# Kernel optimization log

Measured on AMD Instinct MI355X. Metric: run time of the kernel, lower is better.

Reference implementation:

```python
import jax, jax.numpy as jnp
import numpy as np

B, T, L, D, H = 4, 8, 197, 512, 8
DK = D // H
SIM_TH = 0.0
N = T * (L - 1)  # 1568 local tokens

def _ln(x, g, b, eps=1e-5):
    x32 = x.astype(jnp.float32)
    m = jnp.mean(x32, axis=-1, keepdims=True)
    v = jnp.mean((x32 - m) ** 2, axis=-1, keepdims=True)
    return (((x32 - m) * jax.lax.rsqrt(v + eps)) * g + b).astype(x.dtype)

def _qgelu(x):
    return x * jax.nn.sigmoid(1.702 * x)

def _mha(x, w_in, b_in, w_out, b_out):
    # torch nn.MultiheadAttention, x: [S, Bt, D] (seq-first)
    S, Bt, _ = x.shape
    qkv = x @ w_in.T + b_in
    q, k, v = jnp.split(qkv, 3, axis=-1)
    q = q.reshape(S, Bt, H, DK); k = k.reshape(S, Bt, H, DK); v = v.reshape(S, Bt, H, DK)
    scores = jnp.einsum('sbhd,tbhd->bhst', q, k) / jnp.sqrt(jnp.asarray(DK, x.dtype))
    p = jax.nn.softmax(scores, axis=-1)
    o = jnp.einsum('bhst,tbhd->sbhd', p, v).reshape(S, Bt, D)
    return o @ w_out.T + b_out

def _resblock(x, ln1g, ln1b, inw, inb, outw, outb, ln2g, ln2b, fcw, fcb, pw, pb):
    x = x + _mha(_ln(x, ln1g, ln1b), inw, inb, outw, outb)
    h = _qgelu(_ln(x, ln2g, ln2b) @ fcw.T + fcb)
    return x + h @ pw.T + pb

def _build_graph(x, g_mask):
    xd = jax.lax.stop_gradient(x)  # matches x.detach()
    xn = xd / jnp.maximum(jnp.linalg.norm(xd, axis=-1, keepdims=True), 1e-12)
    sim = jnp.einsum('bnd,bmd->bnm', xn, xn)
    adj = jnp.where(sim < SIM_TH, 0.0, sim)
    return adj * g_mask  # t != 1 branch

def _graph_attn(x, mask, wq, bq, wk, bk, wv, bv, wo, bo):
    Bb, Nn, _ = x.shape
    def heads(a):
        return a.reshape(Bb, Nn, H, DK).transpose(0, 2, 1, 3)
    Q = heads(x @ wq.T + bq); K = heads(x @ wk.T + bk); V = heads(x @ wv.T + bv)
    scores = jnp.einsum('bhnd,bhmd->bhnm', Q, K) / jnp.sqrt(jnp.asarray(DK, x.dtype))
    m = mask[:, None]  # [b,1,N,N]
    scores = jnp.where(m == 0, -jnp.inf, scores * m)  # scores*mask then masked_fill(mask==0,-inf)
    p = jax.nn.softmax(scores, axis=-1)
    o = jnp.einsum('bhnm,bhmd->bhnd', p, V).transpose(0, 2, 1, 3).reshape(Bb, Nn, D)
    return o @ wo.T + bo

def _forward(x, proj_w, proj_b,
             m_ln1g, m_ln1b, m_inw, m_inb, m_outw, m_outb,
             m_ln2g, m_ln2b, m_fcw, m_fcb, m_pw, m_pb,
             g_wq, g_bq, g_wk, g_bk, g_wv, g_bv, g_wo, g_bo,
             ln1g, ln1b, a_inw, a_inb, a_outw, a_outb,
             ln2g, ln2b, fcw, fcb, pw, pb, g_mask):
    b, t, l, d = x.shape
    x = x @ proj_w.T + proj_b
    glob = x[:, :, 0, :].transpose(1, 0, 2)  # [t,b,d]
    msg = (m_ln1g, m_ln1b, m_inw, m_inb, m_outw, m_outb, m_ln2g, m_ln2b, m_fcw, m_fcb, m_pw, m_pb)
    glob = _resblock(glob, *msg)
    glob = _resblock(glob, *msg)  # message_attn applied twice (shared weights)
    glob = glob.reshape(1, t, b, d)
    loc = x[:, :, 1:, :].reshape(b, t * (l - 1), d)
    gm = _build_graph(loc, g_mask)
    loc = _graph_attn(loc, gm, g_wq, g_bq, g_wk, g_bk, g_wv, g_bv, g_wo, g_bo)
    loc = loc.reshape(b, t, l - 1, d).transpose(2, 1, 0, 3)  # [l-1,t,b,d]
    y = jnp.concatenate([glob, loc], axis=0).reshape(l, t * b, d)
    y = y + _mha(_ln(y, ln1g, ln1b), a_inw, a_inb, a_outw, a_outb)
    y = y + _qgelu(_ln(y, ln2g, ln2b) @ fcw.T + fcb) @ pw.T + pb
    return y.reshape(l, t, b, d).transpose(2, 1, 0, 3)  # [b,t,l,d]

def setup_inputs() -> dict:
    key = jax.random.key(0)
    ks = jax.random.split(key, 64)
    s = 0.02
    def w(i, shape):
        return jax.random.normal(ks[i], shape, jnp.float32) * s
    ones = jnp.ones((D,), jnp.float32); zeros = jnp.zeros((D,), jnp.float32)
    gm = (jax.random.uniform(ks[60], (N, N)) < 0.5).astype(jnp.float32)
    gm = gm.at[jnp.arange(N), jnp.arange(N)].set(1.0)  # keep self-edges so no row is fully masked
    return dict(
        x=jax.random.normal(ks[0], (B, T, L, D), jnp.float32),
        proj_w=w(1, (D, D)), proj_b=jnp.zeros((D,), jnp.float32),
        m_ln1g=ones, m_ln1b=zeros,
        m_inw=w(2, (3 * D, D)), m_inb=jnp.zeros((3 * D,), jnp.float32),
        m_outw=w(3, (D, D)), m_outb=zeros,
        m_ln2g=ones, m_ln2b=zeros,
        m_fcw=w(4, (4 * D, D)), m_fcb=jnp.zeros((4 * D,), jnp.float32),
        m_pw=w(5, (D, 4 * D)), m_pb=zeros,
        g_wq=w(6, (D, D)), g_bq=zeros, g_wk=w(7, (D, D)), g_bk=zeros,
        g_wv=w(8, (D, D)), g_bv=zeros, g_wo=w(9, (D, D)), g_bo=zeros,
        ln1g=ones, ln1b=zeros,
        a_inw=w(10, (3 * D, D)), a_inb=jnp.zeros((3 * D,), jnp.float32),
        a_outw=w(11, (D, D)), a_outb=zeros,
        ln2g=ones, ln2b=zeros,
        fcw=w(12, (4 * D, D)), fcb=jnp.zeros((4 * D,), jnp.float32),
        pw=w(13, (D, 4 * D)), pb=zeros,
        g_mask=gm,
    )

def reference(x, proj_w, proj_b, m_ln1g, m_ln1b, m_inw, m_inb, m_outw, m_outb,
              m_ln2g, m_ln2b, m_fcw, m_fcb, m_pw, m_pb,
              g_wq, g_bq, g_wk, g_bk, g_wv, g_bv, g_wo, g_bo,
              ln1g, ln1b, a_inw, a_inb, a_outw, a_outb,
              ln2g, ln2b, fcw, fcb, pw, pb, g_mask):
    return _forward(x, proj_w, proj_b, m_ln1g, m_ln1b, m_inw, m_inb, m_outw, m_outb,
                    m_ln2g, m_ln2b, m_fcw, m_fcb, m_pw, m_pb,
                    g_wq, g_bq, g_wk, g_bk, g_wv, g_bv, g_wo, g_bo,
                    ln1g, ln1b, a_inw, a_inb, a_outw, a_outb,
                    ln2g, ln2b, fcw, fcb, pw, pb, g_mask)
```

## Files before the change

kernel.cpp:

```cpp
#include <hip/hip_runtime.h>
#include <hip/hip_bf16.h>

typedef unsigned short u16;
typedef __attribute__((ext_vector_type(8))) short bf16x8;
typedef __attribute__((ext_vector_type(4))) float f32x4;

#define FINF __builtin_huge_valf()

static __device__ __forceinline__ float bf2f(u16 v){ union{unsigned u; float f;} c; c.u = ((unsigned)v)<<16; return c.f; }
static __device__ __forceinline__ u16 f2bf(float f){ union{__hip_bfloat16 h; u16 u;} c; c.h = __float2bfloat16(f); return c.u; }
static __device__ __forceinline__ bf16x8 scale8(bf16x8 v, float s){
  bf16x8 o;
  #pragma unroll
  for (int e=0;e<8;e++) o[e] = (short)f2bf(bf2f((u16)v[e])*s);
  return o;
}

static __device__ __forceinline__ void gload16(const void* g, void* l){
  __builtin_amdgcn_global_load_lds(
      (const __attribute__((address_space(1))) void*)g,
      (__attribute__((address_space(3))) void*)l, 16, 0, 0);
}

#define WAIT_VM0()   { asm volatile("s_waitcnt vmcnt(0)" ::: "memory"); __builtin_amdgcn_sched_barrier(0); }
#define BARRIER()    { __builtin_amdgcn_sched_barrier(0); __builtin_amdgcn_s_barrier(); __builtin_amdgcn_sched_barrier(0); }

struct CvtArgs {
  const float* src[14];
  u16* dst[14];
  int n[14];
};
__global__ __launch_bounds__(256) void cvt_multi(CvtArgs a){
  int seg = blockIdx.y;
  const float* s = a.src[seg]; u16* d = a.dst[seg]; int n = a.n[seg];
  for (int i = (blockIdx.x*256 + threadIdx.x)*4; i < n; i += gridDim.x*256*4){
    float4 v = *(const float4*)(s + i);
    ushort4 o = { f2bf(v.x), f2bf(v.y), f2bf(v.z), f2bf(v.w) };
    *(ushort4*)(d + i) = o;
  }
}

__global__ __launch_bounds__(256) void concat_bias(const float* a, const float* b, const float* c, float* o){
  int i = blockIdx.x*256 + threadIdx.x;
  o[i] = i < 512 ? a[i] : (i < 1024 ? b[i-512] : c[i-1024]);
}

template<int BM, int EPI, int MW>
__global__ __launch_bounds__(256,MW) void gemm_nt(
    const u16* __restrict__ A, const u16* __restrict__ Bw,
    const float* __restrict__ bias, const float* aux, void* out,
    int M, int Nn, int K, int ldc, long aBatch, long bBatch, long cBatch)
{
  constexpr int MI = BM/32;
  constexpr int WSPAN = BM/2;
  __shared__ __align__(16) u16 a_lds[2*BM*64];
  __shared__ __align__(16) u16 b_lds[2*128*64];
  const int z = blockIdx.z;
  const u16* Az = A + (long)z*aBatch;
  const u16* Bz = Bw + (long)z*bBatch;
  const int n0 = blockIdx.x*128, m0 = blockIdx.y*BM;
  const int t = threadIdx.x, lane = t & 63, wave = t >> 6;
  const int wr = wave >> 1, wc = wave & 1;
  const int r = lane & 15, kq = lane >> 4;

  const int srow = t >> 3;
  const int scol = ((t&7)*8) ^ ((srow&7)<<3);
  int rowA[MI], rowB[4];
  #pragma unroll
  for (int i=0;i<MI;i++){ int ga = m0 + i*32 + srow; rowA[i] = ga < M ? ga : M-1; }
  #pragma unroll
  for (int i=0;i<4;i++){ int gb = n0 + i*32 + srow; rowB[i] = gb < Nn ? gb : Nn-1; }

  f32x4 acc[MI][4] = {};
  const int nkt = K >> 6;

  auto STAGE = [&](int kt, int buf){
    const long koff = (long)kt*64 + scol;
    #pragma unroll
    for (int i=0;i<MI;i++)
      gload16(Az + (long)rowA[i]*K + koff, (char*)a_lds + buf*(BM*128) + i*4096 + wave*1024);
    #pragma unroll
    for (int i=0;i<4;i++)
      gload16(Bz + (long)rowB[i]*K + koff, (char*)b_lds + buf*16384 + i*4096 + wave*1024);
  };

  STAGE(0,0);
  WAIT_VM0(); BARRIER();
  for (int kt=0; kt<nkt; kt++){
    const int cur = kt&1;
    if (kt+1 < nkt) STAGE(kt+1, cur^1);
    const u16* al = a_lds + cur*BM*64;
    const u16* bl = b_lds + cur*8192;
    #pragma unroll
    for (int kk=0; kk<2; kk++){
      bf16x8 af[MI], bfr[4];
      #pragma unroll
      for (int i=0;i<MI;i++){
        int rw = wr*WSPAN + i*16 + r;
        af[i] = *(const bf16x8*)&al[rw*64 + ((kk*32 + kq*8) ^ ((rw&7)<<3))];
      }
      #pragma unroll
      for (int j=0;j<4;j++){
        int rw = wc*64 + j*16 + r;
        bfr[j] = *(const bf16x8*)&bl[rw*64 + ((kk*32 + kq*8) ^ ((rw&7)<<3))];
      }
      #pragma unroll
      for (int i=0;i<MI;i++)
        #pragma unroll
        for (int j=0;j<4;j++)
          acc[i][j] = __builtin_amdgcn_mfma_f32_16x16x32_bf16(af[i], bfr[j], acc[i][j], 0,0,0);
    }
    WAIT_VM0(); BARRIER();
  }

  #pragma unroll
  for (int i=0;i<MI;i++){
    #pragma unroll
    for (int j=0;j<4;j++){
      int gcol = n0 + wc*64 + j*16 + r;
      if (gcol >= Nn) continue;
      float bv = bias ? bias[gcol] : 0.f;
      #pragma unroll
      for (int rr=0; rr<4; rr++){
        int grow = m0 + wr*WSPAN + i*16 + kq*4 + rr;
        if (grow >= M) continue;
        float v = acc[i][j][rr] + bv;
        if constexpr (EPI==0){
          ((float*)out)[(long)z*cBatch + (long)grow*ldc + gcol] = v;
        } else if constexpr (EPI==1){
          ((u16*)out)[(long)z*cBatch + (long)grow*ldc + gcol] = f2bf(v);
        } else if constexpr (EPI==2){
          long idx = (long)z*cBatch + (long)grow*ldc + gcol;
          ((float*)out)[idx] = aux[idx] + v;
        } else if constexpr (EPI==3){
          float g = v / (1.f + __expf(-1.702f*v));
          ((u16*)out)[(long)z*cBatch + (long)grow*ldc + gcol] = f2bf(g);
        } else if constexpr (EPI==4){
          float adj = v < 0.f ? 0.f : v;
          float gmv = aux[(long)grow*Nn + gcol];
          ((u16*)out)[(long)z*cBatch + (long)grow*ldc + gcol] = f2bf(adj*gmv);
        } else if constexpr (EPI==5){
          int b = grow/1568, n = grow%1568, tt = n/196, lp = n%196;
          int yrow = (1+lp)*32 + tt*4 + b;
          ((float*)out)[(long)yrow*ldc + gcol] = v;
        } else if constexpr (EPI==6){
          long idx = (long)grow*ldc + gcol;
          int l = grow>>5, rb = grow&31, tt = rb>>2, bb = rb&3;
          ((float*)out)[((long)((bb*8+tt)*197) + l)*512 + gcol] = aux[idx] + v;
        }
      }
    }
  }
}

__global__ __launch_bounds__(256) void transpose_v(
    const u16* __restrict__ src, u16* __restrict__ vt,
    int nrows, long zofs, long nofs, int vcol0, int outld)
{
  __shared__ u16 tile[64][66];
  const int t = threadIdx.x;
  const int nt = blockIdx.x, h = blockIdx.y, z = blockIdx.z;
  const int n0 = nt*64;
  const int rlo = t>>3, c0 = (t&7)*8;
  #pragma unroll
  for (int i=0;i<2;i++){
    int nl = i*32 + rlo;
    int n = n0 + nl; int nc = n < nrows ? n : nrows-1;
    const u16* s = src + (long)z*zofs + (long)nc*nofs + vcol0 + h*64 + c0;
    uint4 v = *(const uint4*)s;
    bool dead = n >= nrows;
    #pragma unroll
    for (int e=0;e<8;e++) tile[nl][c0+e] = dead ? (u16)0 : ((const u16*)&v)[e];
  }
  __syncthreads();
  #pragma unroll
  for (int i=0;i<2;i++){
    int d = i*32 + rlo;
    u16 tmp[8];
    #pragma unroll
    for (int e=0;e<8;e++) tmp[e] = tile[c0+e][d];
    int ncol = n0 + c0;
    if (ncol + 8 <= outld){
      u16* dst = vt + ((long)((z*8+h)*64 + d))*outld + ncol;
      *(uint4*)dst = *(uint4*)tmp;
    }
  }
}

template<bool MASKED>
__global__ __launch_bounds__(256,4) void flash3(
    const u16* __restrict__ QKV, const u16* __restrict__ VT,
    const u16* __restrict__ gmask, u16* __restrict__ Out,
    int nq, int nk, int nqb, long qBatch, long qRow,
    long oBatch, long oRow, long gmBatch, int vtld)
{
  __shared__ __align__(16) u16 k_lds[2*4096];
  __shared__ __align__(16) u16 p_lds[4][1024];
  int h, z, qb;
  if constexpr (MASKED){
    int id = blockIdx.x;
    int a = id>>6, c = id&7; h = (id>>3)&7;
    int G = a*8 + c;
    if (G >= 4*nqb) return;
    z = G / nqb; qb = G % nqb;
  } else {
    qb = blockIdx.x; h = blockIdx.y; z = blockIdx.z;
  }
  const int t = threadIdx.x, lane = t&63, wave = t>>6;
  const int r = lane&15, kq = lane>>4;
  const u16* Qb = QKV + (long)z*qBatch + h*64;
  const u16* Kb = Qb + 512;
  const u16* Vt = VT + (long)(z*8+h)*64*vtld;
  const int qt0 = qb*64;
  const int q0  = qt0 + wave*16;
  const int q   = q0 + r;
  const int qc  = q < nq ? q : nq-1;
  const u16* Gq = MASKED ? (gmask + (long)z*gmBatch + (long)qc*nk) : nullptr;

  bf16x8 qf0, qf1;
  { const u16* qp = Qb + (long)qc*qRow + kq*8;
    qf0 = scale8(*(const bf16x8*)qp, 0.125f);
    qf1 = scale8(*(const bf16x8*)(qp+32), 0.125f); }

  const int srow = t>>3;
  const int scol = ((t&7)*8) ^ ((srow&7)<<3);

  auto stage_k = [&](int kt, int buf){
    #pragma unroll
    for (int i=0;i<2;i++){
      int j = kt*64 + i*32 + srow; if (j > nk-1) j = nk-1;
      gload16(Kb + (long)j*qRow + scol, (char*)k_lds + buf*8192 + i*4096 + wave*1024);
    }
  };

  bf16x8 ONES;
  #pragma unroll
  for (int e=0;e<8;e++) ONES[e] = (short)0x3F80;

  float m_ = -FINF;
  f32x4 o_[4] = {};  f32x4 l_ = {};

  const int nkt = (nk + 63) >> 6;
  stage_k(0,0);
  __syncthreads();
  for (int kt=0; kt<nkt; kt++){
    const int cur = kt&1;
    if (kt+1 < nkt) stage_k(kt+1, cur^1);

    uint4 vfr[2][4];
    #pragma unroll
    for (int c=0;c<2;c++)
      #pragma unroll
      for (int j=0;j<4;j++)
        vfr[c][j] = *(const uint4*)(Vt + (long)(j*16+r)*vtld + kt*64 + c*32 + kq*8);
    ushort4 gv[4];
    if constexpr (MASKED){
      #pragma unroll
      for (int sub=0;sub<4;sub++)
        gv[sub] = *(const ushort4*)(Gq + kt*64 + sub*16 + kq*4);
    }

    const u16* kl = k_lds + cur*4096;
    float p[4][4];
    #pragma unroll
    for (int sub=0; sub<4; sub++){
      int rw = sub*16 + r; int sw = (rw&7)<<3;
      bf16x8 kf0 = *(const bf16x8*)&kl[rw*64 + ((kq*8) ^ sw)];
      bf16x8 kf1 = *(const bf16x8*)&kl[rw*64 + ((32 + kq*8) ^ sw)];
      f32x4 sc = {};
      sc = __builtin_amdgcn_mfma_f32_16x16x32_bf16(kf0, qf0, sc, 0,0,0);
      sc = __builtin_amdgcn_mfma_f32_16x16x32_bf16(kf1, qf1, sc, 0,0,0);
      #pragma unroll
      for (int rr=0;rr<4;rr++){
        float sv = sc[rr];
        int key = kt*64 + sub*16 + kq*4 + rr;
        if constexpr (MASKED){
          u16 g = ((const u16*)&gv[sub])[rr];
          sv = (g == 0 || key >= nk) ? -FINF : sv * bf2f(g);
        } else {
          if (key >= nk) sv = -FINF;
        }
        p[sub][rr] = sv;
      }
    }

    float mx;
    { float a0 = fmaxf(fmaxf(p[0][0],p[0][1]), fmaxf(p[0][2],p[0][3]));
      float a1 = fmaxf(fmaxf(p[1][0],p[1][1]), fmaxf(p[1][2],p[1][3]));
      float a2 = fmaxf(fmaxf(p[2][0],p[2][1]), fmaxf(p[2][2],p[2][3]));
      float a3 = fmaxf(fmaxf(p[3][0],p[3][1]), fmaxf(p[3][2],p[3][3]));
      mx = fmaxf(fmaxf(a0,a1), fmaxf(a2,a3)); }
    mx = fmaxf(mx, __shfl_xor(mx, 16));
    mx = fmaxf(mx, __shfl_xor(mx, 32));
    float mnew = fmaxf(m_, mx);
    float fac = (m_ == -FINF) ? 0.f : __expf(m_ - mnew);
    #pragma unroll
    for (int j=0;j<4;j++){ o_[j][0]*=fac; o_[j][1]*=fac; o_[j][2]*=fac; o_[j][3]*=fac; }
    l_[0]*=fac; l_[1]*=fac; l_[2]*=fac; l_[3]*=fac;
    m_ = mnew;

    #pragma unroll
    for (int sub=0;sub<4;sub++){
      float e0 = (p[sub][0] == -FINF) ? 0.f : __expf(p[sub][0] - mnew);
      float e1 = (p[sub][1] == -FINF) ? 0.f : __expf(p[sub][1] - mnew);
      float e2 = (p[sub][2] == -FINF) ? 0.f : __expf(p[sub][2] - mnew);
      float e3 = (p[sub][3] == -FINF) ? 0.f : __expf(p[sub][3] - mnew);
      unsigned u0, u1;
      asm volatile("v_cvt_pk_bf16_f32 %0, %1, %2" : "=v"(u0) : "v"(e0), "v"(e1));
      asm volatile("v_cvt_pk_bf16_f32 %0, %1, %2" : "=v"(u1) : "v"(e2), "v"(e3));
      uint2 w; w.x = u0; w.y = u1;
      int idx = r*64 + ((sub*16 + kq*4) ^ ((r&7)<<3));
      *(uint2*)&p_lds[wave][idx] = w;
    }

    #pragma unroll
    for (int c=0;c<2;c++){
      bf16x8 pf = *(const bf16x8*)&p_lds[wave][r*64 + ((c*32 + kq*8) ^ ((r&7)<<3))];
      #pragma unroll
      for (int j=0;j<4;j++){
        bf16x8 vf = *(const bf16x8*)&vfr[c][j];
        o_[j] = __builtin_amdgcn_mfma_f32_16x16x32_bf16(vf, pf, o_[j], 0,0,0);
      }
      l_ = __builtin_amdgcn_mfma_f32_16x16x32_bf16(ONES, pf, l_, 0,0,0);
    }
    __syncthreads();
  }

  float inv = l_[0] > 0.f ? 1.f/l_[0] : 0.f;
  if (q < nq){
    #pragma unroll
    for (int j=0;j<4;j++){
      ushort4 ov = { f2bf(o_[j][0]*inv), f2bf(o_[j][1]*inv),
                     f2bf(o_[j][2]*inv), f2bf(o_[j][3]*inv) };
      *(ushort4*)(Out + (long)z*oBatch + (long)q*oRow + h*64 + j*16 + kq*4) = ov;
    }
  }
}

__global__ __launch_bounds__(256) void ln_rows(const float* __restrict__ in,
    const float* __restrict__ g, const float* __restrict__ b, u16* __restrict__ out, int rows)
{
  int wave = threadIdx.x >> 6, lane = threadIdx.x & 63;
  int row = blockIdx.x*4 + wave;
  if (row >= rows) return;
  const float4* x = (const float4*)(in + (long)row*512);
  float4 v0 = x[lane], v1 = x[lane+64];
  float s  = v0.x+v0.y+v0.z+v0.w + v1.x+v1.y+v1.z+v1.w;
  float ss = v0.x*v0.x+v0.y*v0.y+v0.z*v0.z+v0.w*v0.w + v1.x*v1.x+v1.y*v1.y+v1.z*v1.z+v1.w*v1.w;
  #pragma unroll
  for (int d=1; d<64; d<<=1){ s += __shfl_xor(s,d); ss += __shfl_xor(ss,d); }
  float mean = s * (1.f/512.f);
  float var = ss * (1.f/512.f) - mean*mean;
  float rs = rsqrtf(var + 1e-5f);
  const float4* gg = (const float4*)g; const float4* bb = (const float4*)b;
  float4 g0 = gg[lane], g1 = gg[lane+64], b0 = bb[lane], b1 = bb[lane+64];
  u16* o = out + (long)row*512;
  ushort4 o0 = { f2bf((v0.x-mean)*rs*g0.x + b0.x), f2bf((v0.y-mean)*rs*g0.y + b0.y),
                 f2bf((v0.z-mean)*rs*g0.z + b0.z), f2bf((v0.w-mean)*rs*g0.w + b0.w) };
  ushort4 o1 = { f2bf((v1.x-mean)*rs*g1.x + b1.x), f2bf((v1.y-mean)*rs*g1.y + b1.y),
                 f2bf((v1.z-mean)*rs*g1.z + b1.z), f2bf((v1.w-mean)*rs*g1.w + b1.w) };
  *(ushort4*)(o + lane*4) = o0;
  *(ushort4*)(o + 256 + lane*4) = o1;
}

__global__ __launch_bounds__(256) void locprep(const float* __restrict__ y0,
    u16* __restrict__ xn, u16* __restrict__ locb)
{
  int wave = threadIdx.x >> 6, lane = threadIdx.x & 63;
  int rr = blockIdx.x*4 + wave;
  int bb = rr/1568, n = rr%1568, tt = n/196, lp = n%196;
  const float4* x = (const float4*)(y0 + ((long)((bb*8+tt)*197) + 1 + lp)*512);
  float4 v0 = x[lane], v1 = x[lane+64];
  float ss = v0.x*v0.x+v0.y*v0.y+v0.z*v0.z+v0.w*v0.w + v1.x*v1.x+v1.y*v1.y+v1.z*v1.z+v1.w*v1.w;
  #pragma unroll
  for (int d=1; d<64; d<<=1) ss += __shfl_xor(ss,d);
  float sc = 1.f / fmaxf(sqrtf(ss), 1e-12f);
  u16* ox = xn + (long)rr*512;
  u16* ol = locb + (long)rr*512;
  ushort4 a0 = { f2bf(v0.x*sc), f2bf(v0.y*sc), f2bf(v0.z*sc), f2bf(v0.w*sc) };
  ushort4 a1 = { f2bf(v1.x*sc), f2bf(v1.y*sc), f2bf(v1.z*sc), f2bf(v1.w*sc) };
  ushort4 c0 = { f2bf(v0.x), f2bf(v0.y), f2bf(v0.z), f2bf(v0.w) };
  ushort4 c1 = { f2bf(v1.x), f2bf(v1.y), f2bf(v1.z), f2bf(v1.w) };
  *(ushort4*)(ox + lane*4) = a0;  *(ushort4*)(ox + 256 + lane*4) = a1;
  *(ushort4*)(ol + lane*4) = c0;  *(ushort4*)(ol + 256 + lane*4) = c1;
}

__global__ __launch_bounds__(64) void msg_attn(const u16* __restrict__ mqkv, u16* __restrict__ matt){
  __shared__ float q_s[8][64], k_s[8][64], v_s[8][64];
  int bh = blockIdx.x; int bt = bh>>3, h = bh&7;
  int lane = threadIdx.x;
  int row = lane>>3, cc = (lane&7)*8;
  #pragma unroll
  for (int e=0;e<8;e++){
    long base = (long)(row*4 + bt)*1536 + h*64 + cc + e;
    q_s[row][cc+e] = bf2f(mqkv[base]);
    k_s[row][cc+e] = bf2f(mqkv[base + 512]);
    v_s[row][cc+e] = bf2f(mqkv[base + 1024]);
  }
  __syncthreads();
  int q = lane>>3, k = lane&7;
  float s = 0.f;
  #pragma unroll 16
  for (int d=0; d<64; d++) s += q_s[q][d]*k_s[k][d];
  s *= 0.125f;
  float mx = s;
  #pragma unroll
  for (int d=1; d<8; d<<=1) mx = fmaxf(mx, __shfl_xor(mx,d));
  float p = __expf(s - mx), ps = p;
  #pragma unroll
  for (int d=1; d<8; d<<=1) ps += __shfl_xor(ps,d);
  p /= ps;
  for (int d=0; d<64; d++){
    float ov = p * v_s[k][d];
    #pragma unroll
    for (int m=1; m<8; m<<=1) ov += __shfl_xor(ov,m);
    if (k == (d>>3)) matt[(long)(q*4 + bt)*512 + h*64 + d] = f2bf(ov);
  }
}

__global__ __launch_bounds__(256) void gather_glob(const float* __restrict__ y0, float* __restrict__ glob){
  int idx = blockIdx.x*256 + threadIdx.x;
  int orow = idx>>9, d = idx&511;
  int tt = orow>>2, bb = orow&3;
  glob[idx] = y0[((long)(bb*8+tt)*197)*512 + d];
}
__global__ __launch_bounds__(256) void copy32(const float* __restrict__ glob, float* __restrict__ y){
  int idx = blockIdx.x*256 + threadIdx.x;
  y[idx] = glob[idx];
}

extern "C" void kernel_launch(void* const* d_in, const int* in_sizes, int n_in,
                              void* d_out, int out_size, void* d_ws, size_t ws_size,
                              hipStream_t stream)
{
  const float* x      = (const float*)d_in[0];
  const float* proj_w = (const float*)d_in[1];
  const float* proj_b = (const float*)d_in[2];
  const float* m_ln1g = (const float*)d_in[3];
  const float* m_ln1b = (const float*)d_in[4];
  const float* m_inw  = (const float*)d_in[5];
  const float* m_inb  = (const float*)d_in[6];
  const float* m_outw = (const float*)d_in[7];
  const float* m_outb = (const float*)d_in[8];
  const float* m_ln2g = (const float*)d_in[9];
  const float* m_ln2b = (const float*)d_in[10];
  const float* m_fcw  = (const float*)d_in[11];
  const float* m_fcb  = (const float*)d_in[12];
  const float* m_pw   = (const float*)d_in[13];
  const float* m_pb   = (const float*)d_in[14];
  const float* g_wq = (const float*)d_in[15]; const float* g_bq = (const float*)d_in[16];
  const float* g_wk = (const float*)d_in[17]; const float* g_bk = (const float*)d_in[18];
  const float* g_wv = (const float*)d_in[19]; const float* g_bv = (const float*)d_in[20];
  const float* g_wo = (const float*)d_in[21]; const float* g_bo = (const float*)d_in[22];
  const float* ln1g = (const float*)d_in[23]; const float* ln1b = (const float*)d_in[24];
  const float* a_inw = (const float*)d_in[25]; const float* a_inb = (const float*)d_in[26];
  const float* a_outw = (const float*)d_in[27]; const float* a_outb = (const float*)d_in[28];
  const float* ln2g = (const float*)d_in[29]; const float* ln2b = (const float*)d_in[30];
  const float* fcw = (const float*)d_in[31]; const float* fcb = (const float*)d_in[32];
  const float* pw = (const float*)d_in[33]; const float* pb = (const float*)d_in[34];
  const float* g_mask = (const float*)d_in[35];

  if (ws_size < (size_t)99753984) return;

  char* ws = (char*)d_ws;
  u16* WB = (u16*)ws;
  const long WPROJ=0, WMIN=262144, WMOUT=1048576, WMFC=1310720, WMP=2359296,
             WGQ=3407872, WGK=3670016, WGV=3932160, WGO=4194304,
             WAIN=4456448, WAOUT=5242880, WFC=5505024, WP=6553600;
  float* y0   = (float*)(ws + 15204352);
  float* y    = (float*)(ws + 28114944);
  u16* lnbuf  = (u16*)(ws + 41025536);
  u16* vtg    = (u16*)(ws + 41025536);
  u16* locb   = (u16*)(ws + 47480832);
  u16* qkv    = (u16*)(ws + 53903360);
  u16* xb     = (u16*)(ws + 73269248);
  u16* gm     = (u16*)(ws + 73269248);
  u16* vt2    = (u16*)(ws + 73269248);
  u16* hbuf   = (u16*)(ws + 73269248);
  u16* obuf   = (u16*)(ws + 92938240);
  float* glob = (float*)(ws + 99393536);
  u16* mlnb   = (u16*)(ws + 99459072);
  u16* mqkv   = (u16*)(ws + 99491840);
  u16* matt   = (u16*)(ws + 99590144);
  u16* mh     = (u16*)(ws + 99622912);
  float* gbias = (float*)(ws + 99622912);

  CvtArgs ca;
  auto setseg=[&](int i, const float* s, u16* d, int n){ ca.src[i]=s; ca.dst[i]=d; ca.n[i]=n; };
  setseg(0,  x,      xb,       6304*512);
  setseg(1,  proj_w, WB+WPROJ, 262144);
  setseg(2,  m_inw,  WB+WMIN,  786432);
  setseg(3,  m_outw, WB+WMOUT, 262144);
  setseg(4,  m_fcw,  WB+WMFC,  1048576);
  setseg(5,  m_pw,   WB+WMP,   1048576);
  setseg(6,  g_wq,   WB+WGQ,   262144);
  setseg(7,  g_wk,   WB+WGK,   262144);
  setseg(8,  g_wv,   WB+WGV,   262144);
  setseg(9,  g_wo,   WB+WGO,   262144);
  setseg(10, a_inw,  WB+WAIN,  786432);
  setseg(11, a_outw, WB+WAOUT, 262144);
  setseg(12, fcw,    WB+WFC,   1048576);
  setseg(13, pw,     WB+WP,    1048576);
  cvt_multi<<<dim3(128,14), 256, 0, stream>>>(ca);

  gemm_nt<64,0,3><<<dim3(4,99), 256, 0, stream>>>(xb, WB+WPROJ, proj_b, nullptr, y0, 6304,512,512,512, 0,0,0);

  gather_glob<<<64,256,0,stream>>>(y0, glob);

  for (int it=0; it<2; ++it){
    ln_rows<<<8,256,0,stream>>>(glob, m_ln1g, m_ln1b, mlnb, 32);
    gemm_nt<64,1,3><<<dim3(12,1),256,0,stream>>>(mlnb, WB+WMIN, m_inb, nullptr, mqkv, 32,1536,512,1536, 0,0,0);
    msg_attn<<<32,64,0,stream>>>(mqkv, matt);
    gemm_nt<64,2,3><<<dim3(4,1),256,0,stream>>>(matt, WB+WMOUT, m_outb, glob, glob, 32,512,512,512, 0,0,0);
    ln_rows<<<8,256,0,stream>>>(glob, m_ln2g, m_ln2b, mlnb, 32);
    gemm_nt<64,3,3><<<dim3(16,1),256,0,stream>>>(mlnb, WB+WMFC, m_fcb, nullptr, mh, 32,2048,512,2048, 0,0,0);
    gemm_nt<64,2,3><<<dim3(4,1),256,0,stream>>>(mh, WB+WMP, m_pb, glob, glob, 32,512,2048,512, 0,0,0);
  }

  concat_bias<<<6,256,0,stream>>>(g_bq, g_bk, g_bv, gbias);

  locprep<<<1568,256,0,stream>>>(y0, lnbuf, locb);

  gemm_nt<64,4,3><<<dim3(13,25,4),256,0,stream>>>(lnbuf, lnbuf, nullptr, g_mask, gm,
      1568,1568,512,1568, 1568L*512, 1568L*512, 1568L*1568);

  gemm_nt<64,1,3><<<dim3(12,98),256,0,stream>>>(locb, WB+WGQ, gbias, nullptr, qkv, 6272,1536,512,1536, 0,0,0);

  transpose_v<<<dim3(25,8,4),256,0,stream>>>(qkv, vtg, 1568, 1568L*1536, 1536L, 1024, 1568);

  flash3<true><<<832,256,0,stream>>>(qkv, vtg, gm, obuf,
      1568,1568,25, 1568L*1536, 1536, 1568L*512, 512, 1568L*1568, 1568);

  gemm_nt<64,5,3><<<dim3(4,98),256,0,stream>>>(obuf, WB+WGO, g_bo, nullptr, y, 6272,512,512,512, 0,0,0);

  copy32<<<64,256,0,stream>>>(glob, y);

  ln_rows<<<1576,256,0,stream>>>(y, ln1g, ln1b, lnbuf, 6304);
  gemm_nt<64,1,3><<<dim3(12,99),256,0,stream>>>(lnbuf, WB+WAIN, a_inb, nullptr, qkv, 6304,1536,512,1536, 0,0,0);
  transpose_v<<<dim3(4,8,32),256,0,stream>>>(qkv, vt2, 197, 1536L, 32L*1536, 1024, 256);
  flash3<false><<<dim3(4,8,32),256,0,stream>>>(qkv, vt2, nullptr, obuf,
      197,197,4, 1536, 32L*1536, 512, 32L*512, 0, 256);
  gemm_nt<64,2,3><<<dim3(4,99),256,0,stream>>>(obuf, WB+WAOUT, a_outb, y, y, 6304,512,512,512, 0,0,0);

  ln_rows<<<1576,256,0,stream>>>(y, ln2g, ln2b, lnbuf, 6304);
  gemm_nt<64,3,3><<<dim3(16,99),256,0,stream>>>(lnbuf, WB+WFC, fcb, nullptr, hbuf, 6304,2048,512,2048, 0,0,0);
  gemm_nt<64,6,3><<<dim3(4,99),256,0,stream>>>(hbuf, WB+WP, pb, y, (float*)d_out, 6304,512,2048,512, 0,0,0);
}
```

Baseline: 569.5 us.

## Widen flash key tile to 128, skip uniform rescale, retile narrow GEMMs

The flash attention kernel now processes 128 keys per iteration instead of 64, doubling the K LDS buffers and splitting the P·V update into two halves that share one online-softmax max. The accumulator rescale is skipped when no lane's running max grew. In parallel, the N=512 GEMMs and the small message-token GEMMs switch to a 32-row tile with a different pipeline-depth template parameter, doubling grid rows. The aim is fewer loop iterations and barriers in attention and better CU occupancy for the narrow GEMMs, at the cost of more registers and LDS in flash3 (launch bound lowered to 3 blocks per SM).

New measurement: 539.0 us. 5.4% less time.

```diff
diff --git a/kernel.cpp b/kernel.cpp
--- a/kernel.cpp
+++ b/kernel.cpp
@@ -188,13 +188,13 @@
 }
 
 template<bool MASKED>
-__global__ __launch_bounds__(256,4) void flash3(
+__global__ __launch_bounds__(256,3) void flash3(
     const u16* __restrict__ QKV, const u16* __restrict__ VT,
     const u16* __restrict__ gmask, u16* __restrict__ Out,
     int nq, int nk, int nqb, long qBatch, long qRow,
     long oBatch, long oRow, long gmBatch, int vtld)
 {
-  __shared__ __align__(16) u16 k_lds[2*4096];
+  __shared__ __align__(16) u16 k_lds[2*8192];
   __shared__ __align__(16) u16 p_lds[4][1024];
   int h, z, qb;
   if constexpr (MASKED){
@@ -227,9 +227,9 @@
 
   auto stage_k = [&](int kt, int buf){
     #pragma unroll
-    for (int i=0;i<2;i++){
-      int j = kt*64 + i*32 + srow; if (j > nk-1) j = nk-1;
-      gload16(Kb + (long)j*qRow + scol, (char*)k_lds + buf*8192 + i*4096 + wave*1024);
+    for (int i=0;i<4;i++){
+      int j = kt*128 + i*32 + srow; if (j > nk-1) j = nk-1;
+      gload16(Kb + (long)j*qRow + scol, (char*)k_lds + buf*16384 + i*4096 + wave*1024);
     }
   };
 
@@ -240,30 +240,30 @@
   float m_ = -FINF;
   f32x4 o_[4] = {};  f32x4 l_ = {};
 
-  const int nkt = (nk + 63) >> 6;
+  const int nkt = (nk + 127) >> 7;
   stage_k(0,0);
   __syncthreads();
   for (int kt=0; kt<nkt; kt++){
     const int cur = kt&1;
     if (kt+1 < nkt) stage_k(kt+1, cur^1);
 
-    uint4 vfr[2][4];
+    uint4 vfr0[2][4];
     #pragma unroll
     for (int c=0;c<2;c++)
       #pragma unroll
       for (int j=0;j<4;j++)
-        vfr[c][j] = *(const uint4*)(Vt + (long)(j*16+r)*vtld + kt*64 + c*32 + kq*8);
-    ushort4 gv[4];
+        vfr0[c][j] = *(const uint4*)(Vt + (long)(j*16+r)*vtld + kt*128 + c*32 + kq*8);
+    ushort4 gv[8];
     if constexpr (MASKED){
       #pragma unroll
-      for (int sub=0;sub<4;sub++)
-        gv[sub] = *(const ushort4*)(Gq + kt*64 + sub*16 + kq*4);
-    }
-
-    const u16* kl = k_lds + cur*4096;
-    float p[4][4];
-    #pragma unroll
-    for (int sub=0; sub<4; sub++){
+      for (int sub=0;sub<8;sub++)
+        gv[sub] = *(const ushort4*)(Gq + kt*128 + sub*16 + kq*4);
+    }
+
+    const u16* kl = k_lds + cur*8192;
+    float p[8][4];
+    #pragma unroll
+    for (int sub=0; sub<8; sub++){
       int rw = sub*16 + r; int sw = (rw&7)<<3;
       bf16x8 kf0 = *(const bf16x8*)&kl[rw*64 + ((kq*8) ^ sw)];
       bf16x8 kf1 = *(const bf16x8*)&kl[rw*64 + ((32 + kq*8) ^ sw)];
@@ -273,7 +273,7 @@
       #pragma unroll
       for (int rr=0;rr<4;rr++){
         float sv = sc[rr];
-        int key = kt*64 + sub*16 + kq*4 + rr;
+        int key = kt*128 + sub*16 + kq*4 + rr;
         if constexpr (MASKED){
           u16 g = ((const u16*)&gv[sub])[rr];
           sv = (g == 0 || key >= nk) ? -FINF : sv * bf2f(g);
@@ -285,43 +285,58 @@
     }
 
     float mx;
-    { float a0 = fmaxf(fmaxf(p[0][0],p[0][1]), fmaxf(p[0][2],p[0][3]));
-      float a1 = fmaxf(fmaxf(p[1][0],p[1][1]), fmaxf(p[1][2],p[1][3]));
-      float a2 = fmaxf(fmaxf(p[2][0],p[2][1]), fmaxf(p[2][2],p[2][3]));
-      float a3 = fmaxf(fmaxf(p[3][0],p[3][1]), fmaxf(p[3][2],p[3][3]));
-      mx = fmaxf(fmaxf(a0,a1), fmaxf(a2,a3)); }
+    { float a[8];
+      #pragma unroll
+      for (int sub=0;sub<8;sub++)
+        a[sub] = fmaxf(fmaxf(p[sub][0],p[sub][1]), fmaxf(p[sub][2],p[sub][3]));
+      float b0 = fmaxf(fmaxf(a[0],a[1]), fmaxf(a[2],a[3]));
+      float b1 = fmaxf(fmaxf(a[4],a[5]), fmaxf(a[6],a[7]));
+      mx = fmaxf(b0,b1); }
     mx = fmaxf(mx, __shfl_xor(mx, 16));
     mx = fmaxf(mx, __shfl_xor(mx, 32));
     float mnew = fmaxf(m_, mx);
-    float fac = (m_ == -FINF) ? 0.f : __expf(m_ - mnew);
-    #pragma unroll
-    for (int j=0;j<4;j++){ o_[j][0]*=fac; o_[j][1]*=fac; o_[j][2]*=fac; o_[j][3]*=fac; }
-    l_[0]*=fac; l_[1]*=fac; l_[2]*=fac; l_[3]*=fac;
-    m_ = mnew;
-
-    #pragma unroll
-    for (int sub=0;sub<4;sub++){
-      float e0 = (p[sub][0] == -FINF) ? 0.f : __expf(p[sub][0] - mnew);
-      float e1 = (p[sub][1] == -FINF) ? 0.f : __expf(p[sub][1] - mnew);
-      float e2 = (p[sub][2] == -FINF) ? 0.f : __expf(p[sub][2] - mnew);
-      float e3 = (p[sub][3] == -FINF) ? 0.f : __expf(p[sub][3] - mnew);
-      unsigned u0, u1;
-      asm volatile("v_cvt_pk_bf16_f32 %0, %1, %2" : "=v"(u0) : "v"(e0), "v"(e1));
-      asm volatile("v_cvt_pk_bf16_f32 %0, %1, %2" : "=v"(u1) : "v"(e2), "v"(e3));
-      uint2 w; w.x = u0; w.y = u1;
-      int idx = r*64 + ((sub*16 + kq*4) ^ ((r&7)<<3));
-      *(uint2*)&p_lds[wave][idx] = w;
-    }
-
-    #pragma unroll
-    for (int c=0;c<2;c++){
-      bf16x8 pf = *(const bf16x8*)&p_lds[wave][r*64 + ((c*32 + kq*8) ^ ((r&7)<<3))];
-      #pragma unroll
-      for (int j=0;j<4;j++){
-        bf16x8 vf = *(const bf16x8*)&vfr[c][j];
-        o_[j] = __builtin_amdgcn_mfma_f32_16x16x32_bf16(vf, pf, o_[j], 0,0,0);
+    if (__any(mnew > m_)){
+      float fac = (m_ == -FINF) ? 0.f : __expf(m_ - mnew);
+      #pragma unroll
+      for (int j=0;j<4;j++){ o_[j][0]*=fac; o_[j][1]*=fac; o_[j][2]*=fac; o_[j][3]*=fac; }
+      l_[0]*=fac; l_[1]*=fac; l_[2]*=fac; l_[3]*=fac;
+      m_ = mnew;
+    }
+    mnew = m_;
+
+    uint4 vfr1[2][4];
+    #pragma unroll
+    for (int c=0;c<2;c++)
+      #pragma unroll
+      for (int j=0;j<4;j++)
+        vfr1[c][j] = *(const uint4*)(Vt + (long)(j*16+r)*vtld + kt*128 + 64 + c*32 + kq*8);
+
+    #pragma unroll
+    for (int hf=0; hf<2; hf++){
+      #pragma unroll
+      for (int s4=0;s4<4;s4++){
+        int sub = hf*4 + s4;
+        float e0 = (p[sub][0] == -FINF) ? 0.f : __expf(p[sub][0] - mnew);
+        float e1 = (p[sub][1] == -FINF) ? 0.f : __expf(p[sub][1] - mnew);
+        float e2 = (p[sub][2] == -FINF) ? 0.f : __expf(p[sub][2] - mnew);
+        float e3 = (p[sub][3] == -FINF) ? 0.f : __expf(p[sub][3] - mnew);
+        unsigned u0, u1;
+        asm volatile("v_cvt_pk_bf16_f32 %0, %1, %2" : "=v"(u0) : "v"(e0), "v"(e1));
+        asm volatile("v_cvt_pk_bf16_f32 %0, %1, %2" : "=v"(u1) : "v"(e2), "v"(e3));
+        uint2 w; w.x = u0; w.y = u1;
+        int idx = r*64 + ((s4*16 + kq*4) ^ ((r&7)<<3));
+        *(uint2*)&p_lds[wave][idx] = w;
       }
-      l_ = __builtin_amdgcn_mfma_f32_16x16x32_bf16(ONES, pf, l_, 0,0,0);
+      #pragma unroll
+      for (int c=0;c<2;c++){
+        bf16x8 pf = *(const bf16x8*)&p_lds[wave][r*64 + ((c*32 + kq*8) ^ ((r&7)<<3))];
+        #pragma unroll
+        for (int j=0;j<4;j++){
+          bf16x8 vf = hf ? *(const bf16x8*)&vfr1[c][j] : *(const bf16x8*)&vfr0[c][j];
+          o_[j] = __builtin_amdgcn_mfma_f32_16x16x32_bf16(vf, pf, o_[j], 0,0,0);
+        }
+        l_ = __builtin_amdgcn_mfma_f32_16x16x32_bf16(ONES, pf, l_, 0,0,0);
+      }
     }
     __syncthreads();
   }
@@ -503,18 +518,18 @@
   setseg(13, pw,     WB+WP,    1048576);
   cvt_multi<<<dim3(128,14), 256, 0, stream>>>(ca);
 
-  gemm_nt<64,0,3><<<dim3(4,99), 256, 0, stream>>>(xb, WB+WPROJ, proj_b, nullptr, y0, 6304,512,512,512, 0,0,0);
+  gemm_nt<32,0,4><<<dim3(4,197), 256, 0, stream>>>(xb, WB+WPROJ, proj_b, nullptr, y0, 6304,512,512,512, 0,0,0);
 
   gather_glob<<<64,256,0,stream>>>(y0, glob);
 
   for (int it=0; it<2; ++it){
     ln_rows<<<8,256,0,stream>>>(glob, m_ln1g, m_ln1b, mlnb, 32);
-    gemm_nt<64,1,3><<<dim3(12,1),256,0,stream>>>(mlnb, WB+WMIN, m_inb, nullptr, mqkv, 32,1536,512,1536, 0,0,0);
+    gemm_nt<32,1,4><<<dim3(12,1),256,0,stream>>>(mlnb, WB+WMIN, m_inb, nullptr, mqkv, 32,1536,512,1536, 0,0,0);
     msg_attn<<<32,64,0,stream>>>(mqkv, matt);
-    gemm_nt<64,2,3><<<dim3(4,1),256,0,stream>>>(matt, WB+WMOUT, m_outb, glob, glob, 32,512,512,512, 0,0,0);
+    gemm_nt<32,2,4><<<dim3(4,1),256,0,stream>>>(matt, WB+WMOUT, m_outb, glob, glob, 32,512,512,512, 0,0,0);
     ln_rows<<<8,256,0,stream>>>(glob, m_ln2g, m_ln2b, mlnb, 32);
-    gemm_nt<64,3,3><<<dim3(16,1),256,0,stream>>>(mlnb, WB+WMFC, m_fcb, nullptr, mh, 32,2048,512,2048, 0,0,0);
-    gemm_nt<64,2,3><<<dim3(4,1),256,0,stream>>>(mh, WB+WMP, m_pb, glob, glob, 32,512,2048,512, 0,0,0);
+    gemm_nt<32,3,4><<<dim3(16,1),256,0,stream>>>(mlnb, WB+WMFC, m_fcb, nullptr, mh, 32,2048,512,2048, 0,0,0);
+    gemm_nt<32,2,4><<<dim3(4,1),256,0,stream>>>(mh, WB+WMP, m_pb, glob, glob, 32,512,2048,512, 0,0,0);
   }
 
   concat_bias<<<6,256,0,stream>>>(g_bq, g_bk, g_bv, gbias);
@@ -531,7 +546,7 @@
   flash3<true><<<832,256,0,stream>>>(qkv, vtg, gm, obuf,
       1568,1568,25, 1568L*1536, 1536, 1568L*512, 512, 1568L*1568, 1568);
 
-  gemm_nt<64,5,3><<<dim3(4,98),256,0,stream>>>(obuf, WB+WGO, g_bo, nullptr, y, 6272,512,512,512, 0,0,0);
+  gemm_nt<32,5,4><<<dim3(4,196),256,0,stream>>>(obuf, WB+WGO, g_bo, nullptr, y, 6272,512,512,512, 0,0,0);
 
   copy32<<<64,256,0,stream>>>(glob, y);
 
@@ -540,9 +555,9 @@
   transpose_v<<<dim3(4,8,32),256,0,stream>>>(qkv, vt2, 197, 1536L, 32L*1536, 1024, 256);
   flash3<false><<<dim3(4,8,32),256,0,stream>>>(qkv, vt2, nullptr, obuf,
       197,197,4, 1536, 32L*1536, 512, 32L*512, 0, 256);
-  gemm_nt<64,2,3><<<dim3(4,99),256,0,stream>>>(obuf, WB+WAOUT, a_outb, y, y, 6304,512,512,512, 0,0,0);
+  gemm_nt<32,2,4><<<dim3(4,197),256,0,stream>>>(obuf, WB+WAOUT, a_outb, y, y, 6304,512,512,512, 0,0,0);
 
   ln_rows<<<1576,256,0,stream>>>(y, ln2g, ln2b, lnbuf, 6304);
   gemm_nt<64,3,3><<<dim3(16,99),256,0,stream>>>(lnbuf, WB+WFC, fcb, nullptr, hbuf, 6304,2048,512,2048, 0,0,0);
-  gemm_nt<64,6,3><<<dim3(4,99),256,0,stream>>>(hbuf, WB+WP, pb, y, (float*)d_out, 6304,512,2048,512, 0,0,0);
-}
+  gemm_nt<32,6,4><<<dim3(4,197),256,0,stream>>>(hbuf, WB+WP, pb, y, (float*)d_out, 6304,512,2048,512, 0,0,0);
+}
```
